# Optimization experiments

Hardware: AMD Instinct MI355X
Metric: run time of the kernel (lower is better)

Reference implementation:

```python
import jax, jax.numpy as jnp
import numpy as np

N = 20000      # nodes
E = 320000     # edges
G = 64         # graphs in batch
PD = 9         # property input dim (properties='yyyyyyyyy')
KD = 32        # kernel_dim (node feature dim)
MD = 32        # m_dim (message dim)
FF = 32        # fourier_features
NK = 5         # n_kernels
EIN = FF * 2 + KD + 1 + KD * 2  # 161, edge MLP input dim
MLP = 256
EPS = 1e-5


def layer_norm(x, g, b):
    mu = jnp.mean(x, -1, keepdims=True)
    var = jnp.mean((x - mu) ** 2, -1, keepdims=True)
    return (x - mu) * jax.lax.rsqrt(var + EPS) * g + b


def silu(x):
    return x * jax.nn.sigmoid(x)


def setup_inputs() -> dict:
    key = jax.random.key(0)
    ks = jax.random.split(key, 20)
    rn = lambda k, s: jax.random.normal(k, s, dtype=jnp.float32) * 0.1
    inp = {}
    inp["props"] = jax.random.normal(ks[0], (N, PD), dtype=jnp.float32)
    inp["positions"] = jax.random.normal(ks[1], (N, 3), dtype=jnp.float32)
    inp["edge_props"] = jax.random.normal(ks[2], (E, PD), dtype=jnp.float32)
    inp["embed_W"] = rn(ks[3], (PD, KD)); inp["embed_b"] = jnp.zeros((KD,), jnp.float32)
    inp["edge_embed_W"] = rn(ks[4], (PD, KD)); inp["edge_embed_b"] = jnp.zeros((KD,), jnp.float32)
    # per-kernel params stacked over NK
    inp["k_eW1"] = rn(ks[5], (NK, EIN, EIN * 2)); inp["k_eb1"] = jnp.zeros((NK, EIN * 2), jnp.float32)
    inp["k_eW2"] = rn(ks[6], (NK, EIN * 2, MD)); inp["k_eb2"] = jnp.zeros((NK, MD), jnp.float32)
    inp["k_eln_g"] = jnp.ones((NK, MD), jnp.float32); inp["k_eln_b"] = jnp.zeros((NK, MD), jnp.float32)
    inp["k_nln1_g"] = jnp.ones((NK, KD), jnp.float32); inp["k_nln1_b"] = jnp.zeros((NK, KD), jnp.float32)
    inp["k_nln2_g"] = jnp.ones((NK, KD), jnp.float32); inp["k_nln2_b"] = jnp.zeros((NK, KD), jnp.float32)
    inp["k_nW1"] = rn(ks[7], (NK, KD + MD, KD * 2)); inp["k_nb1"] = jnp.zeros((NK, KD * 2), jnp.float32)
    inp["k_nW2"] = rn(ks[8], (NK, KD * 2, KD)); inp["k_nb2"] = jnp.zeros((NK, KD), jnp.float32)
    inp["fnn_W0"] = rn(ks[9], (KD * (NK + 1), MLP)); inp["fnn_b0"] = jnp.zeros((MLP,), jnp.float32)
    inp["fnn_W1"] = rn(ks[10], (MLP, MLP)); inp["fnn_b1"] = jnp.zeros((MLP,), jnp.float32)
    inp["fnn_W2"] = rn(ks[11], (MLP, MLP)); inp["fnn_b2"] = jnp.zeros((MLP,), jnp.float32)
    inp["fnn_W3"] = rn(ks[12], (MLP, 1)); inp["fnn_b3"] = jnp.zeros((1,), jnp.float32)
    inp["edge_index"] = jax.random.randint(ks[13], (2, E), 0, N, dtype=jnp.int64)
    inp["batch"] = jnp.sort(jax.random.randint(ks[14], (N,), 0, G, dtype=jnp.int64))
    return inp


def egnn_forward(props, positions, edge_props, embed_W, embed_b, edge_embed_W, edge_embed_b,
                 k_eW1, k_eb1, k_eW2, k_eb2, k_eln_g, k_eln_b, k_nln1_g, k_nln1_b,
                 k_nln2_g, k_nln2_b, k_nW1, k_nb1, k_nW2, k_nb2,
                 fnn_W0, fnn_b0, fnn_W1, fnn_b1, fnn_W2, fnn_b2, fnn_W3, fnn_b3,
                 edge_index, batch):
    src, dst = edge_index[0], edge_index[1]  # x_j = source, x_i = target (PyG)
    feats = props @ embed_W + embed_b                     # EmbedNCP (properties-only path)
    edge_feats = edge_props @ edge_embed_W + edge_embed_b  # EmbedEdge
    coords = positions
    # coords are never updated, so the distance/fourier features are the same each round
    rel_coords = coords[src] - coords[dst]
    rel_dist = jnp.sum(rel_coords ** 2, -1, keepdims=True)  # [E,1] squared distance
    scales = 2.0 ** jnp.arange(FF, dtype=jnp.float32)
    d = rel_dist / scales                                    # [E,FF]
    fdist = jnp.concatenate([jnp.sin(d), jnp.cos(d), rel_dist], -1)  # [E,2FF+1]
    edge_attr = jnp.concatenate([fdist, edge_feats], -1)     # [E, 2FF+1+KD]
    deg = jax.ops.segment_sum(jnp.ones((E,), feats.dtype), dst, num_segments=N)
    deg = jnp.maximum(deg, 1.0)[:, None]
    feat_list = [feats]
    for k in range(NK):
        h = jnp.concatenate([feats[dst], feats[src], edge_attr], -1)  # [E, EIN]
        h = silu(h @ k_eW1[k] + k_eb1[k])
        m_ij = silu(h @ k_eW2[k] + k_eb2[k])
        m_ij = layer_norm(m_ij, k_eln_g[k], k_eln_b[k])               # edge_norm1
        m_i = jax.ops.segment_sum(m_ij, dst, num_segments=N) / deg    # mean aggregate
        m_i = layer_norm(m_i, k_eln_g[k], k_eln_b[k])                 # edge_norm1 again (as in source)
        hf = layer_norm(feats, k_nln1_g[k], k_nln1_b[k])
        h2 = jnp.concatenate([hf, m_i], -1)
        h2 = silu(h2 @ k_nW1[k] + k_nb1[k])
        h2 = h2 @ k_nW2[k] + k_nb2[k]
        h2 = layer_norm(h2, k_nln2_g[k], k_nln2_b[k])
        feats = feats + h2                                            # residual
        feat_list.append(feats)
    allf = jnp.concatenate(feat_list, -1)                             # [N, KD*(NK+1)]
    gsum = jax.ops.segment_sum(allf, batch, num_segments=G)
    gcnt = jnp.maximum(jax.ops.segment_sum(jnp.ones((N,), allf.dtype), batch, num_segments=G), 1.0)[:, None]
    g = gsum / gcnt                                                   # mean pool per graph
    g = silu(g @ fnn_W0 + fnn_b0)
    g = silu(g @ fnn_W1 + fnn_b1)
    g = silu(g @ fnn_W2 + fnn_b2)
    return g @ fnn_W3 + fnn_b3                                        # [G, 1]


def reference(props, positions, edge_props, embed_W, embed_b, edge_embed_W, edge_embed_b,
              k_eW1, k_eb1, k_eW2, k_eb2, k_eln_g, k_eln_b, k_nln1_g, k_nln1_b,
              k_nln2_g, k_nln2_b, k_nW1, k_nb1, k_nW2, k_nb2,
              fnn_W0, fnn_b0, fnn_W1, fnn_b1, fnn_W2, fnn_b2, fnn_W3, fnn_b3,
              edge_index, batch):
    return egnn_forward(props, positions, edge_props, embed_W, embed_b, edge_embed_W, edge_embed_b,
                        k_eW1, k_eb1, k_eW2, k_eb2, k_eln_g, k_eln_b, k_nln1_g, k_nln1_b,
                        k_nln2_g, k_nln2_b, k_nW1, k_nb1, k_nW2, k_nb2,
                        fnn_W0, fnn_b0, fnn_W1, fnn_b1, fnn_W2, fnn_b2, fnn_W3, fnn_b3,
                        edge_index, batch)
```

## Files before the change

### kernel.cpp

```cpp
#include <hip/hip_runtime.h>
#include <math.h>

#define N_NODES 20000
#define N_EDGES 320000
#define N_GRAPHS 64
#define PD 9
#define KD 32
#define MD 32
#define NK 5
#define EIN 161
#define EIN2 322
#define ALLF (KD*(NK+1))
#define LN_EPS 1e-5f

typedef __attribute__((ext_vector_type(8))) short short8;
typedef __attribute__((ext_vector_type(4))) float f32x4;
typedef __attribute__((ext_vector_type(4))) unsigned u32x4;
typedef __attribute__((ext_vector_type(2))) unsigned u32x2;
typedef __attribute__((ext_vector_type(4))) int i32x4;

__device__ __forceinline__ float silu_f(float x) { return x / (1.f + __expf(-x)); }

__device__ __forceinline__ unsigned short f2bf(float x) {
    union { float f; unsigned u; } v; v.f = x;
    unsigned r = v.u + 0x7FFFu + ((v.u >> 16) & 1u);
    return (unsigned short)(r >> 16);
}

__device__ __forceinline__ unsigned cvt_pk_bf16(float lo, float hi) {
    unsigned r;
    asm("v_cvt_pk_bf16_f32 %0, %1, %2" : "=v"(r) : "v"(lo), "v"(hi));
    return r;
}

__global__ __launch_bounds__(256) void pack_w1_kernel(
    const float* __restrict__ eW1, unsigned short* __restrict__ W1p)
{
    int fid = blockIdx.x * 256 + threadIdx.x;
    if (fid >= NK*21*5*64) return;
    int kk = fid / (21*5*64);
    int r  = fid % (21*5*64);
    int nt = r / (5*64);
    int r2 = r % (5*64);
    int kb = r2 >> 6;
    int l  = r2 & 63;
    int q = l >> 4, el = l & 15;
    int n = 16*nt + el;
    short8 out;
    #pragma unroll
    for (int i = 0; i < 8; ++i) {
        int kp = 32*kb + 8*q + i;
        int orig = (kp < 128) ? kp : kp + 1;
        float v = (n < EIN2) ? eW1[((size_t)kk*EIN + orig)*EIN2 + n] : 0.f;
        out[i] = (short)f2bf(v);
    }
    *(short8*)&W1p[(size_t)fid*8] = out;
}

__global__ __launch_bounds__(256) void pack_w2_kernel(
    const float* __restrict__ eW2, unsigned short* __restrict__ W2p)
{
    int fid = blockIdx.x * 256 + threadIdx.x;
    if (fid >= NK*2*11*64) return;
    int kk = fid / (2*11*64);
    int r  = fid % (2*11*64);
    int nt2 = r / (11*64);
    int r2  = r % (11*64);
    int kb2 = r2 >> 6;
    int l   = r2 & 63;
    int q = l >> 4, el = l & 15;
    int n = 16*nt2 + el;
    short8 out;
    #pragma unroll
    for (int i = 0; i < 8; ++i) {
        int k2 = 32*kb2 + 8*q + i;
        float v = (k2 < EIN2) ? eW2[((size_t)kk*EIN2 + k2)*MD + n] : 0.f;
        out[i] = (short)f2bf(v);
    }
    *(short8*)&W2p[(size_t)fid*8] = out;
}

__global__ __launch_bounds__(256) void pack_nw_kernel(
    const float* __restrict__ nW1, const float* __restrict__ nW2,
    unsigned short* __restrict__ W1A, unsigned short* __restrict__ W2A)
{
    int fid = blockIdx.x * 256 + threadIdx.x;
    const int tot1 = NK*4*2*64;
    const int tot2 = NK*2*2*64;
    if (fid < tot1) {
        int kk = fid / (4*2*64);
        int r  = fid % (4*2*64);
        int mt = r / 128;
        int r2 = r % 128;
        int kb = r2 >> 6;
        int l  = r2 & 63;
        int q = l >> 4, el = l & 15;
        short8 out;
        #pragma unroll
        for (int i = 0; i < 8; ++i)
            out[i] = (short)f2bf(nW1[((size_t)kk*64 + 32*kb + 8*q + i)*64 + 16*mt + el]);
        *(short8*)&W1A[(size_t)fid*8] = out;
    } else if (fid < tot1 + tot2) {
        int f2 = fid - tot1;
        int kk = f2 / (2*2*64);
        int r  = f2 % (2*2*64);
        int mt2 = r / 128;
        int r2  = r % 128;
        int kb  = r2 >> 6;
        int l   = r2 & 63;
        int q = l >> 4, el = l & 15;
        short8 out;
        #pragma unroll
        for (int i = 0; i < 8; ++i)
            out[i] = (short)f2bf(nW2[((size_t)kk*64 + 32*kb + 8*q + i)*32 + 16*mt2 + el]);
        *(short8*)&W2A[(size_t)f2*8] = out;
    }
}

__global__ __launch_bounds__(256) void embed_nodes_kernel(
    const float* __restrict__ props, const float* __restrict__ W,
    const float* __restrict__ b,
    float* __restrict__ feats, unsigned short* __restrict__ feats_bf,
    float* __restrict__ allf)
{
    int t = threadIdx.x;
    int n = blockIdx.x * 8 + (t >> 5);
    int f = t & 31;
    if (n >= N_NODES) return;
    float acc = b[f];
    #pragma unroll
    for (int i = 0; i < PD; ++i) acc += props[n*PD + i] * W[i*KD + f];
    feats[n*KD + f] = acc;
    feats_bf[n*KD + f] = f2bf(acc);
    allf[(size_t)n*ALLF + f] = acc;
}

__global__ __launch_bounds__(256) void edge_prep_kernel(
    const float* __restrict__ edge_props, const float* __restrict__ positions,
    const int* __restrict__ ei, const float* __restrict__ W,
    const float* __restrict__ b, float* __restrict__ rel,
    float* __restrict__ deg, unsigned short* __restrict__ constpack)
{
    __shared__ float ef[64*32];
    __shared__ float rdl[64];
    int t = threadIdx.x;
    int b0 = blockIdx.x;
    int e0 = b0 * 64;

    {
        int e = t >> 2, sub = t & 3;
        float acc[8];
        #pragma unroll
        for (int j = 0; j < 8; ++j) acc[j] = b[sub*8 + j];
        #pragma unroll
        for (int i = 0; i < PD; ++i) {
            float p = edge_props[(size_t)(e0 + e)*PD + i];
            #pragma unroll
            for (int j = 0; j < 8; ++j) acc[j] += p * W[i*KD + sub*8 + j];
        }
        #pragma unroll
        for (int j = 0; j < 8; ++j) ef[e*32 + sub*8 + j] = acc[j];
    }
    if (t < 64) {
        int e = e0 + t;
        int s = ei[e], d = ei[N_EDGES + e];
        float dx = positions[s*3+0] - positions[d*3+0];
        float dy = positions[s*3+1] - positions[d*3+1];
        float dz = positions[s*3+2] - positions[d*3+2];
        float rd = dx*dx + dy*dy + dz*dz;
        rdl[t] = rd;
        rel[e] = rd;
        atomicAdd(&deg[d], 1.f);
    }
    __syncthreads();

    int l = t & 63, w = t >> 6;
    int q = l >> 4, el = l & 15;
    float rd = rdl[16*w + el];
    #pragma unroll
    for (int kbr = 0; kbr < 3; ++kbr) {
        short8 out;
        #pragma unroll
        for (int i = 0; i < 8; ++i) {
            int k = 8*q + i;
            float v;
            if (kbr == 0)      v = sinf(ldexpf(rd, -k));
            else if (kbr == 1) v = cosf(ldexpf(rd, -k));
            else               v = ef[(16*w + el)*32 + k];
            out[i] = (short)f2bf(v);
        }
        *(short8*)&constpack[((((size_t)b0*4 + w)*3 + kbr)*64 + l)*8] = out;
    }
}

__global__ __launch_bounds__(256) void edge_mlp_mfma(
    const unsigned short* __restrict__ feats_bf,
    const unsigned short* __restrict__ constpack,
    const float* __restrict__ rel, const int* __restrict__ ei,
    const unsigned short* __restrict__ W1p, const unsigned short* __restrict__ W2p,
    const float* __restrict__ w1rd, const float* __restrict__ eb1,
    const float* __restrict__ eb2, const float* __restrict__ lg,
    const float* __restrict__ lb, float* __restrict__ msum)
{
    int t = threadIdx.x;
    int b = blockIdx.x;
    int w = t >> 6, l = t & 63, q = l >> 4, el = l & 15;
    int e0 = b * 64;
    int eMine = e0 + 16*w + el;
    int srcn = ei[eMine];
    int dstn = ei[N_EDGES + eMine];
    float rd = rel[eMine];

    short8 a0 = *(const short8*)&feats_bf[(size_t)dstn*KD + 8*q];
    short8 a1 = *(const short8*)&feats_bf[(size_t)srcn*KD + 8*q];
    const unsigned short* cp = &constpack[((size_t)(b*4 + w)*3)*512 + (size_t)l*8];
    short8 a2 = *(const short8*)&cp[0];
    short8 a3 = *(const short8*)&cp[512];
    short8 a4 = *(const short8*)&cp[1024];

    unsigned h1r[44];
    #pragma unroll
    for (int i = 0; i < 44; ++i) h1r[i] = 0u;

    const int sA = 32*(q & 1) + el;
    const int sB = sA + 16;
    const int myp = q >> 1;

    #pragma unroll
    for (int nt = 0; nt < 21; ++nt) {
        f32x4 acc = {0.f, 0.f, 0.f, 0.f};
        const unsigned short* wb = &W1p[(size_t)(nt*5)*512 + (size_t)l*8];
        acc = __builtin_amdgcn_mfma_f32_16x16x32_bf16(*(const short8*)&wb[0],    a0, acc, 0, 0, 0);
        acc = __builtin_amdgcn_mfma_f32_16x16x32_bf16(*(const short8*)&wb[512],  a1, acc, 0, 0, 0);
        acc = __builtin_amdgcn_mfma_f32_16x16x32_bf16(*(const short8*)&wb[1024], a2, acc, 0, 0, 0);
        acc = __builtin_amdgcn_mfma_f32_16x16x32_bf16(*(const short8*)&wb[1536], a3, acc, 0, 0, 0);
        acc = __builtin_amdgcn_mfma_f32_16x16x32_bf16(*(const short8*)&wb[2048], a4, acc, 0, 0, 0);

        float vj[4];
        if (nt < 20) {
            f32x4 be = *(const f32x4*)&eb1[16*nt + 4*q];
            f32x4 wr = *(const f32x4*)&w1rd[16*nt + 4*q];
            #pragma unroll
            for (int j = 0; j < 4; ++j)
                vj[j] = silu_f(acc[j] + be[j] + rd * wr[j]);
        } else {
            int nb = 320 + 4*q;
            #pragma unroll
            for (int j = 0; j < 4; ++j) {
                int n1 = nb + j;
                bool ok = n1 < EIN2;
                float be = ok ? eb1[n1] : 0.f;
                float wr = ok ? w1rd[n1] : 0.f;
                float v = silu_f(acc[j] + be + rd * wr);
                vj[j] = ok ? v : 0.f;
            }
        }

        unsigned P0 = cvt_pk_bf16(vj[0], vj[1]);
        unsigned P1 = cvt_pk_bf16(vj[2], vj[3]);
        unsigned g0 = (unsigned)__shfl((int)P0, sA);
        unsigned g1 = (unsigned)__shfl((int)P1, sA);
        unsigned g2 = (unsigned)__shfl((int)P0, sB);
        unsigned g3 = (unsigned)__shfl((int)P1, sB);
        const int kb2 = nt >> 1;
        bool recv = (myp == (nt & 1));
        h1r[kb2*4+0] = recv ? g0 : h1r[kb2*4+0];
        h1r[kb2*4+1] = recv ? g1 : h1r[kb2*4+1];
        h1r[kb2*4+2] = recv ? g2 : h1r[kb2*4+2];
        h1r[kb2*4+3] = recv ? g3 : h1r[kb2*4+3];
    }

    f32x4 acc20 = {0.f, 0.f, 0.f, 0.f};
    f32x4 acc21 = {0.f, 0.f, 0.f, 0.f};
    #pragma unroll
    for (int kb2 = 0; kb2 < 11; ++kb2) {
        u32x4 hv = { h1r[kb2*4+0], h1r[kb2*4+1], h1r[kb2*4+2], h1r[kb2*4+3] };
        short8 av = __builtin_bit_cast(short8, hv);
        short8 b0 = *(const short8*)&W2p[(size_t)kb2*512 + (size_t)l*8];
        short8 b1 = *(const short8*)&W2p[(size_t)(11 + kb2)*512 + (size_t)l*8];
        acc20 = __builtin_amdgcn_mfma_f32_16x16x32_bf16(av, b0, acc20, 0, 0, 0);
        acc21 = __builtin_amdgcn_mfma_f32_16x16x32_bf16(av, b1, acc21, 0, 0, 0);
    }

    i32x4 dstv = *(const i32x4*)&ei[N_EDGES + e0 + 16*w + 4*q];
    float e20 = eb2[el], e21 = eb2[16 + el];
    float g0v = lg[el],  g1v = lg[16 + el];
    float b0v = lb[el],  b1v = lb[16 + el];
    #pragma unroll
    for (int j = 0; j < 4; ++j) {
        float m0 = silu_f(acc20[j] + e20);
        float m1 = silu_f(acc21[j] + e21);
        float s = m0 + m1;
        s += __shfl_xor(s, 1, 16); s += __shfl_xor(s, 2, 16);
        s += __shfl_xor(s, 4, 16); s += __shfl_xor(s, 8, 16);
        float mu = s * (1.f/32.f);
        float d0 = m0 - mu, d1 = m1 - mu;
        float vv = d0*d0 + d1*d1;
        vv += __shfl_xor(vv, 1, 16); vv += __shfl_xor(vv, 2, 16);
        vv += __shfl_xor(vv, 4, 16); vv += __shfl_xor(vv, 8, 16);
        float rs = rsqrtf(vv * (1.f/32.f) + LN_EPS);
        int dst = dstv[j];
        atomicAdd(&msum[(size_t)dst*MD + el],      d0*rs*g0v + b0v);
        atomicAdd(&msum[(size_t)dst*MD + 16 + el], d1*rs*g1v + b1v);
    }
}

__global__ __launch_bounds__(256) void node_mlp_mfma(
    const float* __restrict__ msum, const float* __restrict__ deg,
    const unsigned short* __restrict__ W1A, const unsigned short* __restrict__ W2A,
    const float* __restrict__ nb1, const float* __restrict__ nb2,
    const float* __restrict__ eln_g, const float* __restrict__ eln_b,
    const float* __restrict__ n1g, const float* __restrict__ n1b,
    const float* __restrict__ n2g, const float* __restrict__ n2b,
    float* __restrict__ feats, unsigned short* __restrict__ feats_bf,
    float* __restrict__ allf, int kslot)
{
    int t = threadIdx.x;
    int w = t >> 6, l = t & 63, q = l >> 4, el = l & 15;
    int nd = blockIdx.x*64 + 16*w + el;
    bool okn = nd < N_NODES;
    size_t ndc = okn ? (size_t)nd : (size_t)(N_NODES - 1);

    float x[2][8];
    {
        f32x4 f0 = *(const f32x4*)&feats[ndc*KD + 8*q];
        f32x4 f1 = *(const f32x4*)&feats[ndc*KD + 8*q + 4];
        float inv = 1.f / fmaxf(deg[ndc], 1.f);
        f32x4 m0 = *(const f32x4*)&msum[ndc*KD + 8*q];
        f32x4 m1 = *(const f32x4*)&msum[ndc*KD + 8*q + 4];
        #pragma unroll
        for (int j = 0; j < 4; ++j) {
            x[0][j] = f0[j]; x[0][4+j] = f1[j];
            x[1][j] = m0[j]*inv; x[1][4+j] = m1[j]*inv;
        }
    }
    short8 xf[2];
    #pragma unroll
    for (int kb = 0; kb < 2; ++kb) {
        float s = 0.f;
        #pragma unroll
        for (int i = 0; i < 8; ++i) s += x[kb][i];
        s += __shfl_xor(s, 16); s += __shfl_xor(s, 32);
        float mu = s * (1.f/32.f);
        float vv = 0.f;
        #pragma unroll
        for (int i = 0; i < 8; ++i) { float d = x[kb][i] - mu; vv += d*d; }
        vv += __shfl_xor(vv, 16); vv += __shfl_xor(vv, 32);
        float rs = rsqrtf(vv * (1.f/32.f) + LN_EPS);
        const float* gp = kb ? eln_g : n1g;
        const float* bp = kb ? eln_b : n1b;
        f32x4 ga = *(const f32x4*)&gp[8*q];
        f32x4 gb = *(const f32x4*)&gp[8*q + 4];
        f32x4 ba = *(const f32x4*)&bp[8*q];
        f32x4 bb = *(const f32x4*)&bp[8*q + 4];
        float z[8];
        #pragma unroll
        for (int j = 0; j < 4; ++j) {
            z[j]   = (x[kb][j]   - mu)*rs*ga[j] + ba[j];
            z[4+j] = (x[kb][4+j] - mu)*rs*gb[j] + bb[j];
        }
        u32x4 pv = { cvt_pk_bf16(z[0], z[1]), cvt_pk_bf16(z[2], z[3]),
                     cvt_pk_bf16(z[4], z[5]), cvt_pk_bf16(z[6], z[7]) };
        xf[kb] = __builtin_bit_cast(short8, pv);
    }

    const int sA = 32*(q & 1) + el;
    const int sB = sA + 16;
    const int myp = q >> 1;
    unsigned hr[8];
    #pragma unroll
    for (int i = 0; i < 8; ++i) hr[i] = 0u;

    #pragma unroll
    for (int mt = 0; mt < 4; ++mt) {
        f32x4 acc = {0.f, 0.f, 0.f, 0.f};
        acc = __builtin_amdgcn_mfma_f32_16x16x32_bf16(
            *(const short8*)&W1A[(size_t)(mt*2 + 0)*512 + (size_t)l*8], xf[0], acc, 0, 0, 0);
        acc = __builtin_amdgcn_mfma_f32_16x16x32_bf16(
            *(const short8*)&W1A[(size_t)(mt*2 + 1)*512 + (size_t)l*8], xf[1], acc, 0, 0, 0);
        f32x4 b1v = *(const f32x4*)&nb1[16*mt + 4*q];
        float vj[4];
        #pragma unroll
        for (int j = 0; j < 4; ++j) vj[j] = silu_f(acc[j] + b1v[j]);
        unsigned P0 = cvt_pk_bf16(vj[0], vj[1]);
        unsigned P1 = cvt_pk_bf16(vj[2], vj[3]);
        unsigned g0 = (unsigned)__shfl((int)P0, sA);
        unsigned g1 = (unsigned)__shfl((int)P1, sA);
        unsigned g2 = (unsigned)__shfl((int)P0, sB);
        unsigned g3 = (unsigned)__shfl((int)P1, sB);
        const int kb2 = mt >> 1;
        bool recv = (myp == (mt & 1));
        hr[kb2*4+0] = recv ? g0 : hr[kb2*4+0];
        hr[kb2*4+1] = recv ? g1 : hr[kb2*4+1];
        hr[kb2*4+2] = recv ? g2 : hr[kb2*4+2];
        hr[kb2*4+3] = recv ? g3 : hr[kb2*4+3];
    }

    u32x4 h0v = { hr[0], hr[1], hr[2], hr[3] };
    u32x4 h1v = { hr[4], hr[5], hr[6], hr[7] };
    short8 hf0 = __builtin_bit_cast(short8, h0v);
    short8 hf1 = __builtin_bit_cast(short8, h1v);
    float o[2][4];
    #pragma unroll
    for (int mt2 = 0; mt2 < 2; ++mt2) {
        f32x4 acc = {0.f, 0.f, 0.f, 0.f};
        acc = __builtin_amdgcn_mfma_f32_16x16x32_bf16(
            *(const short8*)&W2A[(size_t)(mt2*2 + 0)*512 + (size_t)l*8], hf0, acc, 0, 0, 0);
        acc = __builtin_amdgcn_mfma_f32_16x16x32_bf16(
            *(const short8*)&W2A[(size_t)(mt2*2 + 1)*512 + (size_t)l*8], hf1, acc, 0, 0, 0);
        f32x4 b2v = *(const f32x4*)&nb2[16*mt2 + 4*q];
        #pragma unroll
        for (int j = 0; j < 4; ++j) o[mt2][j] = acc[j] + b2v[j];
    }
    float s2 = 0.f;
    #pragma unroll
    for (int mt2 = 0; mt2 < 2; ++mt2)
        #pragma unroll
        for (int j = 0; j < 4; ++j) s2 += o[mt2][j];
    s2 += __shfl_xor(s2, 16); s2 += __shfl_xor(s2, 32);
    float mu2 = s2 * (1.f/32.f);
    float vv2 = 0.f;
    #pragma unroll
    for (int mt2 = 0; mt2 < 2; ++mt2)
        #pragma unroll
        for (int j = 0; j < 4; ++j) { float d = o[mt2][j] - mu2; vv2 += d*d; }
    vv2 += __shfl_xor(vv2, 16); vv2 += __shfl_xor(vv2, 32);
    float rs2 = rsqrtf(vv2 * (1.f/32.f) + LN_EPS);

    #pragma unroll
    for (int mt2 = 0; mt2 < 2; ++mt2) {
        f32x4 gv = *(const f32x4*)&n2g[16*mt2 + 4*q];
        f32x4 bv = *(const f32x4*)&n2b[16*mt2 + 4*q];
        f32x4 fold = *(const f32x4*)&feats[ndc*KD + 16*mt2 + 4*q];
        f32x4 nf;
        #pragma unroll
        for (int j = 0; j < 4; ++j)
            nf[j] = fold[j] + (o[mt2][j] - mu2)*rs2*gv[j] + bv[j];
        if (okn) {
            *(f32x4*)&feats[(size_t)nd*KD + 16*mt2 + 4*q] = nf;
            u32x2 pb = { cvt_pk_bf16(nf[0], nf[1]), cvt_pk_bf16(nf[2], nf[3]) };
            *(u32x2*)&feats_bf[(size_t)nd*KD + 16*mt2 + 4*q] = pb;
            *(f32x4*)&allf[(size_t)nd*ALLF + kslot*KD + 16*mt2 + 4*q] = nf;
        }
    }
}

__global__ __launch_bounds__(256) void pool_kernel(
    const float* __restrict__ allf, const int* __restrict__ batch,
    float* __restrict__ gsum, float* __restrict__ gcnt)
{
    int b = blockIdx.x, t = threadIdx.x;
    int g = b >> 2, part = b & 3;
    int lo = 0, hi = N_NODES;
    while (lo < hi) { int m = (lo+hi) >> 1; if (batch[m] < g) lo = m+1; else hi = m; }
    int start = lo;
    hi = N_NODES;
    while (lo < hi) { int m = (lo+hi) >> 1; if (batch[m] < g+1) lo = m+1; else hi = m; }
    int end = lo;
    if (part == 0 && t == 0) gcnt[g] = (float)(end - start);
    int len = end - start;
    int chunk = (len + 3) >> 2;
    int s = start + part*chunk;
    int e = min(end, s + chunk);
    if (t < ALLF && e > s) {
        float acc = 0.f;
        for (int n = s; n < e; ++n) acc += allf[(size_t)n*ALLF + t];
        atomicAdd(&gsum[g*ALLF + t], acc);
    }
}

__global__ __launch_bounds__(256) void fnn_kernel(
    const float* __restrict__ gsum, const float* __restrict__ gcnt,
    const float* __restrict__ W0, const float* __restrict__ b0,
    const float* __restrict__ W1, const float* __restrict__ b1,
    const float* __restrict__ W2, const float* __restrict__ b2,
    const float* __restrict__ W3, const float* __restrict__ b3,
    float* __restrict__ out)
{
    __shared__ float xs[256];
    __shared__ float partial[4];
    int g = blockIdx.x, t = threadIdx.x;
    float inv = 1.f / fmaxf(gcnt[g], 1.f);
    if (t < ALLF) xs[t] = gsum[g*ALLF + t] * inv;
    __syncthreads();
    float acc = b0[t];
    for (int i = 0; i < ALLF; ++i) acc += xs[i] * W0[i*256 + t];
    acc = silu_f(acc);
    __syncthreads(); xs[t] = acc; __syncthreads();
    acc = b1[t];
    for (int i = 0; i < 256; ++i) acc += xs[i] * W1[i*256 + t];
    acc = silu_f(acc);
    __syncthreads(); xs[t] = acc; __syncthreads();
    acc = b2[t];
    for (int i = 0; i < 256; ++i) acc += xs[i] * W2[i*256 + t];
    acc = silu_f(acc);
    __syncthreads(); xs[t] = acc; __syncthreads();
    float v = xs[t] * W3[t];
    #pragma unroll
    for (int m = 32; m; m >>= 1) v += __shfl_xor(v, m, 64);
    if ((t & 63) == 0) partial[t >> 6] = v;
    __syncthreads();
    if (t == 0) out[g] = partial[0] + partial[1] + partial[2] + partial[3] + b3[0];
}

extern "C" void kernel_launch(void* const* d_in, const int* in_sizes, int n_in,
                              void* d_out, int out_size, void* d_ws, size_t ws_size,
                              hipStream_t stream) {
    const float* props      = (const float*)d_in[0];
    const float* positions  = (const float*)d_in[1];
    const float* edge_props = (const float*)d_in[2];
    const float* embed_W    = (const float*)d_in[3];
    const float* embed_b    = (const float*)d_in[4];
    const float* eeW        = (const float*)d_in[5];
    const float* eeb        = (const float*)d_in[6];
    const float* k_eW1      = (const float*)d_in[7];
    const float* k_eb1      = (const float*)d_in[8];
    const float* k_eW2      = (const float*)d_in[9];
    const float* k_eb2      = (const float*)d_in[10];
    const float* k_eln_g    = (const float*)d_in[11];
    const float* k_eln_b    = (const float*)d_in[12];
    const float* k_n1g      = (const float*)d_in[13];
    const float* k_n1b      = (const float*)d_in[14];
    const float* k_n2g      = (const float*)d_in[15];
    const float* k_n2b      = (const float*)d_in[16];
    const float* k_nW1      = (const float*)d_in[17];
    const float* k_nb1      = (const float*)d_in[18];
    const float* k_nW2      = (const float*)d_in[19];
    const float* k_nb2      = (const float*)d_in[20];
    const float* fnn_W0     = (const float*)d_in[21];
    const float* fnn_b0     = (const float*)d_in[22];
    const float* fnn_W1     = (const float*)d_in[23];
    const float* fnn_b1     = (const float*)d_in[24];
    const float* fnn_W2     = (const float*)d_in[25];
    const float* fnn_b2     = (const float*)d_in[26];
    const float* fnn_W3     = (const float*)d_in[27];
    const float* fnn_b3     = (const float*)d_in[28];
    const int*   ei         = (const int*)d_in[29];
    const int*   batch      = (const int*)d_in[30];
    float* out = (float*)d_out;

    char* wsb = (char*)d_ws;
    size_t off = 0;
    #define WS_ALLOC(ptr_t, name, bytes) ptr_t name = (ptr_t)(wsb + off); off += (((size_t)(bytes)) + 255) & ~(size_t)255;
    WS_ALLOC(float*, feats, (size_t)N_NODES*KD*4)
    WS_ALLOC(float*, msum,  (size_t)N_NODES*KD*4)
    WS_ALLOC(float*, deg,   (size_t)N_NODES*4)
    WS_ALLOC(float*, rel,   (size_t)N_EDGES*4)
    WS_ALLOC(float*, gsum,  (size_t)N_GRAPHS*ALLF*4)
    WS_ALLOC(float*, gcnt,  (size_t)N_GRAPHS*4)
    WS_ALLOC(float*, allf,  (size_t)N_NODES*ALLF*4)
    WS_ALLOC(unsigned short*, feats_bf,  (size_t)N_NODES*KD*2)
    WS_ALLOC(unsigned short*, constpack, (size_t)5000*4*3*64*8*2)
    WS_ALLOC(unsigned short*, W1p,  (size_t)NK*21*5*64*8*2)
    WS_ALLOC(unsigned short*, W2p,  (size_t)NK*2*11*64*8*2)
    WS_ALLOC(unsigned short*, W1An, (size_t)NK*4*2*64*8*2)
    WS_ALLOC(unsigned short*, W2An, (size_t)NK*2*2*64*8*2)
    (void)ws_size;

    hipMemsetAsync(deg,  0, (size_t)N_NODES*4, stream);
    hipMemsetAsync(gsum, 0, (size_t)N_GRAPHS*ALLF*4, stream);

    pack_w1_kernel<<<(NK*21*5*64 + 255)/256, 256, 0, stream>>>(k_eW1, W1p);
    pack_w2_kernel<<<(NK*2*11*64 + 255)/256, 256, 0, stream>>>(k_eW2, W2p);
    pack_nw_kernel<<<(NK*4*2*64 + NK*2*2*64 + 255)/256, 256, 0, stream>>>(k_nW1, k_nW2, W1An, W2An);
    embed_nodes_kernel<<<N_NODES/8, 256, 0, stream>>>(props, embed_W, embed_b,
                                                      feats, feats_bf, allf);
    edge_prep_kernel<<<N_EDGES/64, 256, 0, stream>>>(edge_props, positions, ei, eeW, eeb,
                                                     rel, deg, constpack);

    for (int k = 0; k < NK; ++k) {
        hipMemsetAsync(msum, 0, (size_t)N_NODES*KD*4, stream);
        edge_mlp_mfma<<<N_EDGES/64, 256, 0, stream>>>(
            feats_bf, constpack, rel, ei,
            W1p + (size_t)k*21*5*512, W2p + (size_t)k*2*11*512,
            k_eW1 + (size_t)k*EIN*EIN2 + 128*EIN2,
            k_eb1 + (size_t)k*EIN2, k_eb2 + (size_t)k*MD,
            k_eln_g + (size_t)k*MD, k_eln_b + (size_t)k*MD, msum);
        node_mlp_mfma<<<(N_NODES + 63)/64, 256, 0, stream>>>(
            msum, deg,
            W1An + (size_t)k*4*2*512, W2An + (size_t)k*2*2*512,
            k_nb1 + (size_t)k*64, k_nb2 + (size_t)k*32,
            k_eln_g + (size_t)k*MD, k_eln_b + (size_t)k*MD,
            k_n1g + (size_t)k*KD, k_n1b + (size_t)k*KD,
            k_n2g + (size_t)k*KD, k_n2b + (size_t)k*KD,
            feats, feats_bf, allf, k+1);
    }

    pool_kernel<<<N_GRAPHS*4, 256, 0, stream>>>(allf, batch, gsum, gcnt);
    fnn_kernel<<<N_GRAPHS, 256, 0, stream>>>(gsum, gcnt, fnn_W0, fnn_b0, fnn_W1, fnn_b1,
                                             fnn_W2, fnn_b2, fnn_W3, fnn_b3, out);
}
```

Before: 882.3 us.

## Permute packed W1 column order so MFMA outputs feed next layer without shuffles

The packed first-layer weights (edge and node MLPs) are reordered so each lane's MFMA output rows line up directly with the B-operand layout of the second GEMM. This removes the cross-lane shuffles and the 44-register hidden buffer. The second-layer MFMAs are interleaved into the first-layer loop, and the five-step accumulation chain is split into two independent accumulators to shorten dependency latency. This relies on the permuted index mapping matching the MFMA operand layout exactly, including the padded last tile.

```diff
diff --git a/kernel.cpp b/kernel.cpp
--- a/kernel.cpp
+++ b/kernel.cpp
@@ -45,7 +45,7 @@
     int kb = r2 >> 6;
     int l  = r2 & 63;
     int q = l >> 4, el = l & 15;
-    int n = 16*nt + el;
+    int n = 32*(nt >> 1) + 8*(el >> 2) + 4*(nt & 1) + (el & 3);
     short8 out;
     #pragma unroll
     for (int i = 0; i < 8; ++i) {
@@ -95,10 +95,11 @@
         int kb = r2 >> 6;
         int l  = r2 & 63;
         int q = l >> 4, el = l & 15;
+        int n = 32*(mt >> 1) + 8*(el >> 2) + 4*(mt & 1) + (el & 3);
         short8 out;
         #pragma unroll
         for (int i = 0; i < 8; ++i)
-            out[i] = (short)f2bf(nW1[((size_t)kk*64 + 32*kb + 8*q + i)*64 + 16*mt + el]);
+            out[i] = (short)f2bf(nW1[((size_t)kk*64 + 32*kb + 8*q + i)*64 + n]);
         *(short8*)&W1A[(size_t)fid*8] = out;
     } else if (fid < tot1 + tot2) {
         int f2 = fid - tot1;
@@ -218,66 +219,61 @@
     short8 a3 = *(const short8*)&cp[512];
     short8 a4 = *(const short8*)&cp[1024];
 
-    unsigned h1r[44];
-    #pragma unroll
-    for (int i = 0; i < 44; ++i) h1r[i] = 0u;
-
-    const int sA = 32*(q & 1) + el;
-    const int sB = sA + 16;
-    const int myp = q >> 1;
+    f32x4 acc20 = {0.f, 0.f, 0.f, 0.f};
+    f32x4 acc21 = {0.f, 0.f, 0.f, 0.f};
+    unsigned pk0 = 0u, pk1 = 0u, pk2 = 0u, pk3 = 0u;
 
     #pragma unroll
     for (int nt = 0; nt < 21; ++nt) {
-        f32x4 acc = {0.f, 0.f, 0.f, 0.f};
+        f32x4 aA = {0.f, 0.f, 0.f, 0.f};
+        f32x4 aB = {0.f, 0.f, 0.f, 0.f};
         const unsigned short* wb = &W1p[(size_t)(nt*5)*512 + (size_t)l*8];
-        acc = __builtin_amdgcn_mfma_f32_16x16x32_bf16(*(const short8*)&wb[0],    a0, acc, 0, 0, 0);
-        acc = __builtin_amdgcn_mfma_f32_16x16x32_bf16(*(const short8*)&wb[512],  a1, acc, 0, 0, 0);
-        acc = __builtin_amdgcn_mfma_f32_16x16x32_bf16(*(const short8*)&wb[1024], a2, acc, 0, 0, 0);
-        acc = __builtin_amdgcn_mfma_f32_16x16x32_bf16(*(const short8*)&wb[1536], a3, acc, 0, 0, 0);
-        acc = __builtin_amdgcn_mfma_f32_16x16x32_bf16(*(const short8*)&wb[2048], a4, acc, 0, 0, 0);
-
+        aA = __builtin_amdgcn_mfma_f32_16x16x32_bf16(*(const short8*)&wb[0],    a0, aA, 0, 0, 0);
+        aA = __builtin_amdgcn_mfma_f32_16x16x32_bf16(*(const short8*)&wb[512],  a1, aA, 0, 0, 0);
+        aA = __builtin_amdgcn_mfma_f32_16x16x32_bf16(*(const short8*)&wb[1024], a2, aA, 0, 0, 0);
+        aB = __builtin_amdgcn_mfma_f32_16x16x32_bf16(*(const short8*)&wb[1536], a3, aB, 0, 0, 0);
+        aB = __builtin_amdgcn_mfma_f32_16x16x32_bf16(*(const short8*)&wb[2048], a4, aB, 0, 0, 0);
+
+        int base = 32*(nt >> 1) + 4*(nt & 1) + 8*q;
         float vj[4];
         if (nt < 20) {
-            f32x4 be = *(const f32x4*)&eb1[16*nt + 4*q];
-            f32x4 wr = *(const f32x4*)&w1rd[16*nt + 4*q];
+            f32x4 be = *(const f32x4*)&eb1[base];
+            f32x4 wr = *(const f32x4*)&w1rd[base];
             #pragma unroll
             for (int j = 0; j < 4; ++j)
-                vj[j] = silu_f(acc[j] + be[j] + rd * wr[j]);
+                vj[j] = silu_f(aA[j] + aB[j] + be[j] + rd * wr[j]);
         } else {
-            int nb = 320 + 4*q;
             #pragma unroll
             for (int j = 0; j < 4; ++j) {
-                int n1 = nb + j;
+                int n1 = base + j;
                 bool ok = n1 < EIN2;
                 float be = ok ? eb1[n1] : 0.f;
                 float wr = ok ? w1rd[n1] : 0.f;
-                float v = silu_f(acc[j] + be + rd * wr);
+                float v = silu_f(aA[j] + aB[j] + be + rd * wr);
                 vj[j] = ok ? v : 0.f;
             }
         }
 
-        unsigned P0 = cvt_pk_bf16(vj[0], vj[1]);
-        unsigned P1 = cvt_pk_bf16(vj[2], vj[3]);
-        unsigned g0 = (unsigned)__shfl((int)P0, sA);
-        unsigned g1 = (unsigned)__shfl((int)P1, sA);
-        unsigned g2 = (unsigned)__shfl((int)P0, sB);
-        unsigned g3 = (unsigned)__shfl((int)P1, sB);
-        const int kb2 = nt >> 1;
-        bool recv = (myp == (nt & 1));
-        h1r[kb2*4+0] = recv ? g0 : h1r[kb2*4+0];
-        h1r[kb2*4+1] = recv ? g1 : h1r[kb2*4+1];
-        h1r[kb2*4+2] = recv ? g2 : h1r[kb2*4+2];
-        h1r[kb2*4+3] = recv ? g3 : h1r[kb2*4+3];
-    }
-
-    f32x4 acc20 = {0.f, 0.f, 0.f, 0.f};
-    f32x4 acc21 = {0.f, 0.f, 0.f, 0.f};
-    #pragma unroll
-    for (int kb2 = 0; kb2 < 11; ++kb2) {
-        u32x4 hv = { h1r[kb2*4+0], h1r[kb2*4+1], h1r[kb2*4+2], h1r[kb2*4+3] };
+        if ((nt & 1) == 0) {
+            pk0 = cvt_pk_bf16(vj[0], vj[1]);
+            pk1 = cvt_pk_bf16(vj[2], vj[3]);
+        } else {
+            pk2 = cvt_pk_bf16(vj[0], vj[1]);
+            pk3 = cvt_pk_bf16(vj[2], vj[3]);
+            const int kb2 = nt >> 1;
+            u32x4 hv = { pk0, pk1, pk2, pk3 };
+            short8 av = __builtin_bit_cast(short8, hv);
+            short8 b0 = *(const short8*)&W2p[(size_t)kb2*512 + (size_t)l*8];
+            short8 b1 = *(const short8*)&W2p[(size_t)(11 + kb2)*512 + (size_t)l*8];
+            acc20 = __builtin_amdgcn_mfma_f32_16x16x32_bf16(av, b0, acc20, 0, 0, 0);
+            acc21 = __builtin_amdgcn_mfma_f32_16x16x32_bf16(av, b1, acc21, 0, 0, 0);
+        }
+    }
+    {
+        u32x4 hv = { pk0, pk1, 0u, 0u };
         short8 av = __builtin_bit_cast(short8, hv);
-        short8 b0 = *(const short8*)&W2p[(size_t)kb2*512 + (size_t)l*8];
-        short8 b1 = *(const short8*)&W2p[(size_t)(11 + kb2)*512 + (size_t)l*8];
+        short8 b0 = *(const short8*)&W2p[(size_t)10*512 + (size_t)l*8];
+        short8 b1 = *(const short8*)&W2p[(size_t)21*512 + (size_t)l*8];
         acc20 = __builtin_amdgcn_mfma_f32_16x16x32_bf16(av, b0, acc20, 0, 0, 0);
         acc21 = __builtin_amdgcn_mfma_f32_16x16x32_bf16(av, b1, acc21, 0, 0, 0);
     }
@@ -364,13 +360,7 @@
         xf[kb] = __builtin_bit_cast(short8, pv);
     }
 
-    const int sA = 32*(q & 1) + el;
-    const int sB = sA + 16;
-    const int myp = q >> 1;
     unsigned hr[8];
-    #pragma unroll
-    for (int i = 0; i < 8; ++i) hr[i] = 0u;
-
     #pragma unroll
     for (int mt = 0; mt < 4; ++mt) {
         f32x4 acc = {0.f, 0.f, 0.f, 0.f};
@@ -378,22 +368,14 @@
             *(const short8*)&W1A[(size_t)(mt*2 + 0)*512 + (size_t)l*8], xf[0], acc, 0, 0, 0);
         acc = __builtin_amdgcn_mfma_f32_16x16x32_bf16(
             *(const short8*)&W1A[(size_t)(mt*2 + 1)*512 + (size_t)l*8], xf[1], acc, 0, 0, 0);
-        f32x4 b1v = *(const f32x4*)&nb1[16*mt + 4*q];
+        int base = 32*(mt >> 1) + 4*(mt & 1) + 8*q;
+        f32x4 b1v = *(const f32x4*)&nb1[base];
         float vj[4];
         #pragma unroll
         for (int j = 0; j < 4; ++j) vj[j] = silu_f(acc[j] + b1v[j]);
-        unsigned P0 = cvt_pk_bf16(vj[0], vj[1]);
-        unsigned P1 = cvt_pk_bf16(vj[2], vj[3]);
-        unsigned g0 = (unsigned)__shfl((int)P0, sA);
-        unsigned g1 = (unsigned)__shfl((int)P1, sA);
-        unsigned g2 = (unsigned)__shfl((int)P0, sB);
-        unsigned g3 = (unsigned)__shfl((int)P1, sB);
-        const int kb2 = mt >> 1;
-        bool recv = (myp == (mt & 1));
-        hr[kb2*4+0] = recv ? g0 : hr[kb2*4+0];
-        hr[kb2*4+1] = recv ? g1 : hr[kb2*4+1];
-        hr[kb2*4+2] = recv ? g2 : hr[kb2*4+2];
-        hr[kb2*4+3] = recv ? g3 : hr[kb2*4+3];
+        int ix = (mt >> 1)*4 + (mt & 1)*2;
+        hr[ix]     = cvt_pk_bf16(vj[0], vj[1]);
+        hr[ix + 1] = cvt_pk_bf16(vj[2], vj[3]);
     }
 
     u32x4 h0v = { hr[0], hr[1], hr[2], hr[3] };
```

Result: faster. 829.8 us (-6.0%).
